# Performance work log

Measured on AMD Instinct MI355X. Metric: run time of the kernel, lower is better.

The kernel has to match this reference:

```python
import jax, jax.numpy as jnp
import numpy as np

B, T, F, H = 64, 512, 512, 1024


def setup_inputs() -> dict:
    key = jax.random.key(0)
    k1, k2, k3 = jax.random.split(key, 3)
    x = jax.random.normal(k1, (B, T, F), dtype=jnp.float32)
    c0 = jnp.zeros((B, H), dtype=jnp.float32)
    h0 = jnp.zeros((B, H), dtype=jnp.float32)
    # Flax LSTMCell: input projection (no bias) + hidden projection (with bias),
    # fused here into [4H]-wide kernels with gate order (i, f, g, o).
    Wi = jax.random.normal(k2, (F, 4 * H), dtype=jnp.float32) / np.sqrt(F)
    Wh = jax.random.normal(k3, (H, 4 * H), dtype=jnp.float32) / np.sqrt(H)
    bh = jnp.zeros((4 * H,), dtype=jnp.float32)
    return {"x": x, "c0": c0, "h0": h0, "Wi": Wi, "Wh": Wh, "bh": bh}


def reference(x, c0, h0, Wi, Wh, bh):
    # Precompute input projections for the whole sequence in one big GEMM.
    # zx: (T, B, 4H)
    zx = jnp.einsum('btf,fg->tbg', x, Wi)

    def step(carry, zx_t):
        c, h = carry
        z = zx_t + h @ Wh + bh  # (B, 4H)
        i, f, g, o = jnp.split(z, 4, axis=-1)
        i = jax.nn.sigmoid(i)
        f = jax.nn.sigmoid(f)
        g = jnp.tanh(g)
        o = jax.nn.sigmoid(o)
        c_new = f * c + i * g
        h_new = o * jnp.tanh(c_new)
        return (c_new, h_new), h_new

    (_, _), ys = jax.lax.scan(step, (c0, h0), zx)
    return jnp.swapaxes(ys, 0, 1)  # (B, T, H)
```

## Files before the change

kernel.cpp:

```cpp
#include <hip/hip_runtime.h>

#define Bdim 64
#define Tdim 512
#define Fdim 512
#define Hdim 1024
#define NKB  48
#define NXKB 16
#define NHKB 32
#define NWG  128
#define NTHR 256

typedef __attribute__((ext_vector_type(8))) _Float16     f16x8;
typedef __attribute__((ext_vector_type(4))) float        f32x4;
typedef __attribute__((ext_vector_type(4))) unsigned int u32x4;

#define MFMA(a, b, c) __builtin_amdgcn_mfma_f32_16x16x32_f16((a), (b), (c), 0, 0, 0)

#define WP_ELEMS    (256*48*64*8)
#define BIAS_OFF    ((size_t)WP_ELEMS * 2)
#define HBUF_OFF    (BIAS_OFF + 4096 * 4)
#define SLOT_BYTES  131072
#define NRING       513
#define FLAG_OFF    (HBUF_OFF + (size_t)NRING * SLOT_BYTES)
#define FLAG_STRIDE 32

__device__ __forceinline__ float sigmoidf_(float v) {
    return 1.0f / (1.0f + __expf(-v));
}
__device__ __forceinline__ float tanhf_(float v) {
    return 1.0f - 2.0f / (1.0f + __expf(2.0f * v));
}

__device__ __forceinline__ f16x8 uload16_l2(const void* p) {
    f16x8 r;
    asm volatile("global_load_dwordx4 %0, %1, off sc0"
                 : "=v"(r) : "v"(p) : "memory");
    return r;
}
__device__ __forceinline__ void ustore16(void* p, f32x4 v) {
    asm volatile("global_store_dwordx4 %0, %1, off sc0 sc1"
                 :: "v"(p), "v"(v) : "memory");
}

#define WAITV(N) do { asm volatile("s_waitcnt vmcnt(" #N ")" ::: "memory"); \
                      __builtin_amdgcn_sched_barrier(0); } while (0)

__global__ void pack_w_kernel(const float* __restrict__ Wi, const float* __restrict__ Wh,
                              _Float16* __restrict__ Wp)
{
    int d = blockIdx.x * blockDim.x + threadIdx.x;
    int tn   = d / 3072;
    int r    = d % 3072;
    int kb   = r / 64;
    int lane = r % 64;
    int kg = lane >> 4, lm = lane & 15;
    int Np = tn * 16 + lm;
    int g    = Np >> 5;
    int lc   = Np & 31;
    int gate = lc >> 3, c = lc & 7;
    int n  = gate * Hdim + g * 8 + c;
    int k0 = kb * 32 + kg * 8;
    f16x8 v;
#pragma unroll
    for (int j = 0; j < 8; ++j) {
        int k = k0 + j;
        float w = (k < Fdim) ? Wi[(long)k * 4096 + n] : Wh[(long)(k - Fdim) * 4096 + n];
        v[j] = (_Float16)w;
    }
    ((f16x8*)Wp)[d] = v;
}

__global__ void pack_misc_kernel(const float* __restrict__ bh, const float* __restrict__ h0,
                                 float* __restrict__ bias_p, _Float16* __restrict__ hbuf,
                                 unsigned int* __restrict__ flags)
{
    int t = blockIdx.x * blockDim.x + threadIdx.x;
    if (t < NWG) flags[t * FLAG_STRIDE] = 0u;
    if (t < 4096) {
        int g = t >> 5, lc = t & 31;
        int gate = lc >> 3, c = lc & 7;
        bias_p[t] = bh[gate * Hdim + g * 8 + c];
    }
    {
        int wgp = t >> 9;
        int b   = (t >> 3) & 63;
        int c   = t & 7;
        hbuf[t] = (_Float16)h0[b * Hdim + wgp * 8 + c];
    }
}

__global__ __launch_bounds__(NTHR, 1)
void lstm_kernel(const float* __restrict__ x, const float* __restrict__ c0,
                 const f16x8* __restrict__ Wp8, const float* __restrict__ bias_p,
                 _Float16* __restrict__ hbuf, unsigned int* __restrict__ flags,
                 float* __restrict__ out)
{
    __shared__ f16x8 wlds[2 * NKB * 64];
    __shared__ float zlds[Bdim][33];

    const int wg   = (blockIdx.x & 7) * 16 + (blockIdx.x >> 3);
    const int tid  = threadIdx.x;
    const int wave = tid >> 6;
    const int lane = tid & 63;
    const int kg = lane >> 4;
    const int lm = lane & 15;

    {
        const f16x8* src = Wp8 + (size_t)wg * 2 * NKB * 64;
        for (int e = tid; e < 2 * NKB * 64; e += NTHR) wlds[e] = src[e];
    }

    const float bias0 = bias_p[wg * 32 + lm];
    const float bias1 = bias_p[wg * 32 + 16 + lm];

    const int grow = wave * 16 + (lane >> 2);
    const int gjl  = (lane & 3) * 2;
    float cc0 = c0[grow * Hdim + wg * 8 + gjl];
    float cc1 = c0[grow * Hdim + wg * 8 + gjl + 1];

    const int arow = wave * 16 + lm;
    const float* __restrict__ xrow = x + (size_t)arow * Tdim * Fdim + kg * 8;

    char* __restrict__ hb  = (char*)hbuf;
    const char* __restrict__ hrd = hb + (size_t)kg * 1024 + (size_t)arow * 16;
    const size_t mypkt = (size_t)wg * 1024 + (size_t)grow * 16;

    __syncthreads();

    for (int t = 0; t < Tdim; ++t) {
        const unsigned int gen = (unsigned int)t;

        f32x4 acc0a = {bias0, bias0, bias0, bias0};
        f32x4 acc1a = {bias1, bias1, bias1, bias1};
        f32x4 acc0b = {0.f, 0.f, 0.f, 0.f};
        f32x4 acc1b = {0.f, 0.f, 0.f, 0.f};

        {
            const float* xt = xrow + (size_t)t * Fdim;
#pragma unroll 8
            for (int kb = 0; kb < NXKB; ++kb) {
                const f32x4* ap = (const f32x4*)(xt + kb * 32);
                f32x4 lo = ap[0];
                f32x4 hi = ap[1];
                f16x8 a;
#pragma unroll
                for (int j = 0; j < 4; ++j) { a[j] = (_Float16)lo[j]; a[4 + j] = (_Float16)hi[j]; }
                f16x8 bf0 = wlds[kb * 64 + lane];
                f16x8 bf1 = wlds[NKB * 64 + kb * 64 + lane];
                if (kb & 1) { acc0b = MFMA(a, bf0, acc0b); acc1b = MFMA(a, bf1, acc1b); }
                else        { acc0a = MFMA(a, bf0, acc0a); acc1a = MFMA(a, bf1, acc1a); }
            }
        }

        if (t && wave == 0) {
            const unsigned int target = 4u * gen;
            while (true) {
                unsigned int f0 = __hip_atomic_load(flags + (size_t)lane * FLAG_STRIDE,
                                                    __ATOMIC_RELAXED, __HIP_MEMORY_SCOPE_AGENT);
                unsigned int f1 = __hip_atomic_load(flags + (size_t)(64 + lane) * FLAG_STRIDE,
                                                    __ATOMIC_RELAXED, __HIP_MEMORY_SCOPE_AGENT);
                if (__all(f0 >= target && f1 >= target)) break;
                __builtin_amdgcn_s_sleep(1);
            }
        }
        __syncthreads();

        {
            const char* hq = hrd + (size_t)t * SLOT_BYTES;
            f16x8 hA[8], hB[8];

#define HLOAD(BASE, H)                                                  \
            _Pragma("unroll")                                           \
            for (int k = 0; k < 8; ++k)                                 \
                H[k] = uload16_l2(hq + (size_t)((BASE) + k) * 4096);

#define HGROUP(BASE, H)                                                 \
            _Pragma("unroll")                                           \
            for (int k = 0; k < 8; ++k) {                               \
                int kb = (BASE) + k;                                    \
                f16x8 bf0 = wlds[(NXKB + kb) * 64 + lane];              \
                f16x8 bf1 = wlds[NKB * 64 + (NXKB + kb) * 64 + lane];   \
                if (kb & 1) { acc0b = MFMA(H[k], bf0, acc0b); acc1b = MFMA(H[k], bf1, acc1b); } \
                else        { acc0a = MFMA(H[k], bf0, acc0a); acc1a = MFMA(H[k], bf1, acc1a); } \
            }

            HLOAD(0,  hA);
            HLOAD(8,  hB);
            WAITV(8);
            HGROUP(0,  hA);
            HLOAD(16, hA);
            WAITV(8);
            HGROUP(8,  hB);
            HLOAD(24, hB);
            WAITV(8);
            HGROUP(16, hA);
            WAITV(0);
            HGROUP(24, hB);
#undef HLOAD
#undef HGROUP
        }
        f32x4 z0 = acc0a + acc0b;
        f32x4 z1 = acc1a + acc1b;

        {
            int rbase = wave * 16 + kg * 4;
#pragma unroll
            for (int r = 0; r < 4; ++r) {
                zlds[rbase + r][lm]      = z0[r];
                zlds[rbase + r][16 + lm] = z1[r];
            }
        }
        asm volatile("s_waitcnt lgkmcnt(0)" ::: "memory");
        __builtin_amdgcn_sched_barrier(0);

        float hv0, hv1;
        {
            float i0 = sigmoidf_(zlds[grow][gjl]);
            float f0 = sigmoidf_(zlds[grow][8 + gjl]);
            float g0 = tanhf_(zlds[grow][16 + gjl]);
            float o0 = sigmoidf_(zlds[grow][24 + gjl]);
            cc0 = f0 * cc0 + i0 * g0;
            hv0 = o0 * tanhf_(cc0);

            float i1 = sigmoidf_(zlds[grow][gjl + 1]);
            float f1 = sigmoidf_(zlds[grow][8 + gjl + 1]);
            float g1 = tanhf_(zlds[grow][16 + gjl + 1]);
            float o1 = sigmoidf_(zlds[grow][24 + gjl + 1]);
            cc1 = f1 * cc1 + i1 * g1;
            hv1 = o1 * tanhf_(cc1);
        }

        {
            union { _Float16 h[2]; unsigned int u; } pk;
            pk.h[0] = (_Float16)hv0; pk.h[1] = (_Float16)hv1;
            const int lb = lane & ~3;
            unsigned int q0 = __shfl(pk.u, lb);
            unsigned int q1 = __shfl(pk.u, lb + 1);
            unsigned int q2 = __shfl(pk.u, lb + 2);
            unsigned int q3 = __shfl(pk.u, lb + 3);
            if (!(lane & 3)) {
                u32x4 pkt = {q0, q1, q2, q3};
                ustore16(hb + (size_t)(t + 1) * SLOT_BYTES + mypkt,
                         __builtin_bit_cast(f32x4, pkt));
            }
        }
        asm volatile("s_waitcnt vmcnt(0)" ::: "memory");
        if (lane == 0)
            __hip_atomic_fetch_add(flags + (size_t)wg * FLAG_STRIDE, 1u,
                                   __ATOMIC_RELAXED, __HIP_MEMORY_SCOPE_AGENT);

        {
            float2 ov; ov.x = hv0; ov.y = hv1;
            *(float2*)(out + ((size_t)grow * Tdim + t) * Hdim + wg * 8 + gjl) = ov;
        }
    }
}

extern "C" void kernel_launch(void* const* d_in, const int* in_sizes, int n_in,
                              void* d_out, int out_size, void* d_ws, size_t ws_size,
                              hipStream_t stream)
{
    const float* x  = (const float*)d_in[0];
    const float* c0 = (const float*)d_in[1];
    const float* h0 = (const float*)d_in[2];
    const float* Wi = (const float*)d_in[3];
    const float* Wh = (const float*)d_in[4];
    const float* bh = (const float*)d_in[5];
    float* out = (float*)d_out;

    char* ws = (char*)d_ws;
    _Float16*     Wp     = (_Float16*)(ws);
    float*        bias_p = (float*)(ws + BIAS_OFF);
    _Float16*     hbuf   = (_Float16*)(ws + HBUF_OFF);
    unsigned int* flags  = (unsigned int*)(ws + FLAG_OFF);

    hipLaunchKernelGGL(pack_w_kernel,    dim3(3072), dim3(256), 0, stream, Wi, Wh, Wp);
    hipLaunchKernelGGL(pack_misc_kernel, dim3(256),  dim3(256), 0, stream, bh, h0, bias_p, hbuf, flags);
    hipLaunchKernelGGL(lstm_kernel, dim3(NWG), dim3(NTHR), 0, stream,
                       x, c0, (const f16x8*)Wp, bias_p, hbuf, flags, out);
}
```

Baseline: 3.380 ms.

## Split each workgroup's gate tiles across eight waves instead of four

Workgroup size goes from 256 to 512 threads. Each wave now computes one 16-column gate tile for a 16-row block, rather than both tiles, so the serial MFMA chain per wave each timestep is halved. The gate nonlinearities are remapped to one hidden unit per lane, and an added barrier covers the cross-wave exchange through shared memory. The completion-flag target becomes 8 per step to match the wave count. In exchange, the x and h fragments are now loaded by two waves each, and there is an extra workgroup barrier every timestep.

```diff
diff --git a/kernel.cpp b/kernel.cpp
--- a/kernel.cpp
+++ b/kernel.cpp
@@ -8,7 +8,7 @@
 #define NXKB 16
 #define NHKB 32
 #define NWG  128
-#define NTHR 256
+#define NTHR 512
 
 typedef __attribute__((ext_vector_type(8))) _Float16     f16x8;
 typedef __attribute__((ext_vector_type(4))) float        f32x4;
@@ -98,27 +98,28 @@
     __shared__ f16x8 wlds[2 * NKB * 64];
     __shared__ float zlds[Bdim][33];
 
-    const int wg   = (blockIdx.x & 7) * 16 + (blockIdx.x >> 3);
-    const int tid  = threadIdx.x;
-    const int wave = tid >> 6;
-    const int lane = tid & 63;
-    const int kg = lane >> 4;
-    const int lm = lane & 15;
+    const int wg    = (blockIdx.x & 7) * 16 + (blockIdx.x >> 3);
+    const int tid   = threadIdx.x;
+    const int wave  = tid >> 6;
+    const int lane  = tid & 63;
+    const int kg    = lane >> 4;
+    const int lm    = lane & 15;
+    const int rtile = wave >> 1;
+    const int ctile = wave & 1;
 
     {
         const f16x8* src = Wp8 + (size_t)wg * 2 * NKB * 64;
         for (int e = tid; e < 2 * NKB * 64; e += NTHR) wlds[e] = src[e];
     }
 
-    const float bias0 = bias_p[wg * 32 + lm];
-    const float bias1 = bias_p[wg * 32 + 16 + lm];
-
-    const int grow = wave * 16 + (lane >> 2);
-    const int gjl  = (lane & 3) * 2;
-    float cc0 = c0[grow * Hdim + wg * 8 + gjl];
-    float cc1 = c0[grow * Hdim + wg * 8 + gjl + 1];
-
-    const int arow = wave * 16 + lm;
+    const float bias = bias_p[wg * 32 + ctile * 16 + lm];
+    const int   woff = ctile * (NKB * 64);
+
+    const int grow = wave * 8 + (lane >> 3);
+    const int gcol = lane & 7;
+    float cc = c0[grow * Hdim + wg * 8 + gcol];
+
+    const int arow = rtile * 16 + lm;
     const float* __restrict__ xrow = x + (size_t)arow * Tdim * Fdim + kg * 8;
 
     char* __restrict__ hb  = (char*)hbuf;
@@ -130,10 +131,8 @@
     for (int t = 0; t < Tdim; ++t) {
         const unsigned int gen = (unsigned int)t;
 
-        f32x4 acc0a = {bias0, bias0, bias0, bias0};
-        f32x4 acc1a = {bias1, bias1, bias1, bias1};
-        f32x4 acc0b = {0.f, 0.f, 0.f, 0.f};
-        f32x4 acc1b = {0.f, 0.f, 0.f, 0.f};
+        f32x4 acca = {bias, bias, bias, bias};
+        f32x4 accb = {0.f, 0.f, 0.f, 0.f};
 
         {
             const float* xt = xrow + (size_t)t * Fdim;
@@ -145,15 +144,14 @@
                 f16x8 a;
 #pragma unroll
                 for (int j = 0; j < 4; ++j) { a[j] = (_Float16)lo[j]; a[4 + j] = (_Float16)hi[j]; }
-                f16x8 bf0 = wlds[kb * 64 + lane];
-                f16x8 bf1 = wlds[NKB * 64 + kb * 64 + lane];
-                if (kb & 1) { acc0b = MFMA(a, bf0, acc0b); acc1b = MFMA(a, bf1, acc1b); }
-                else        { acc0a = MFMA(a, bf0, acc0a); acc1a = MFMA(a, bf1, acc1a); }
+                f16x8 bf = wlds[woff + kb * 64 + lane];
+                if (kb & 1) accb = MFMA(a, bf, accb);
+                else        acca = MFMA(a, bf, acca);
             }
         }
 
         if (t && wave == 0) {
-            const unsigned int target = 4u * gen;
+            const unsigned int target = 8u * gen;
             while (true) {
                 unsigned int f0 = __hip_atomic_load(flags + (size_t)lane * FLAG_STRIDE,
                                                     __ATOMIC_RELAXED, __HIP_MEMORY_SCOPE_AGENT);
@@ -163,7 +161,7 @@
                 __builtin_amdgcn_s_sleep(1);
             }
         }
-        __syncthreads();
+        __builtin_amdgcn_s_barrier();
 
         {
             const char* hq = hrd + (size_t)t * SLOT_BYTES;
@@ -178,10 +176,9 @@
             _Pragma("unroll")                                           \
             for (int k = 0; k < 8; ++k) {                               \
                 int kb = (BASE) + k;                                    \
-                f16x8 bf0 = wlds[(NXKB + kb) * 64 + lane];              \
-                f16x8 bf1 = wlds[NKB * 64 + (NXKB + kb) * 64 + lane];   \
-                if (kb & 1) { acc0b = MFMA(H[k], bf0, acc0b); acc1b = MFMA(H[k], bf1, acc1b); } \
-                else        { acc0a = MFMA(H[k], bf0, acc0a); acc1a = MFMA(H[k], bf1, acc1a); } \
+                f16x8 bf = wlds[woff + (NXKB + kb) * 64 + lane];        \
+                if (kb & 1) accb = MFMA(H[k], bf, accb);                \
+                else        acca = MFMA(H[k], bf, acca);                \
             }
 
             HLOAD(0,  hA);
@@ -199,46 +196,37 @@
 #undef HLOAD
 #undef HGROUP
         }
-        f32x4 z0 = acc0a + acc0b;
-        f32x4 z1 = acc1a + acc1b;
-
-        {
-            int rbase = wave * 16 + kg * 4;
+        f32x4 z = acca + accb;
+
+        {
+            int rbase = rtile * 16 + kg * 4;
 #pragma unroll
-            for (int r = 0; r < 4; ++r) {
-                zlds[rbase + r][lm]      = z0[r];
-                zlds[rbase + r][16 + lm] = z1[r];
-            }
+            for (int r = 0; r < 4; ++r)
+                zlds[rbase + r][ctile * 16 + lm] = z[r];
         }
         asm volatile("s_waitcnt lgkmcnt(0)" ::: "memory");
-        __builtin_amdgcn_sched_barrier(0);
-
-        float hv0, hv1;
-        {
-            float i0 = sigmoidf_(zlds[grow][gjl]);
-            float f0 = sigmoidf_(zlds[grow][8 + gjl]);
-            float g0 = tanhf_(zlds[grow][16 + gjl]);
-            float o0 = sigmoidf_(zlds[grow][24 + gjl]);
-            cc0 = f0 * cc0 + i0 * g0;
-            hv0 = o0 * tanhf_(cc0);
-
-            float i1 = sigmoidf_(zlds[grow][gjl + 1]);
-            float f1 = sigmoidf_(zlds[grow][8 + gjl + 1]);
-            float g1 = tanhf_(zlds[grow][16 + gjl + 1]);
-            float o1 = sigmoidf_(zlds[grow][24 + gjl + 1]);
-            cc1 = f1 * cc1 + i1 * g1;
-            hv1 = o1 * tanhf_(cc1);
-        }
-
-        {
-            union { _Float16 h[2]; unsigned int u; } pk;
-            pk.h[0] = (_Float16)hv0; pk.h[1] = (_Float16)hv1;
-            const int lb = lane & ~3;
-            unsigned int q0 = __shfl(pk.u, lb);
-            unsigned int q1 = __shfl(pk.u, lb + 1);
-            unsigned int q2 = __shfl(pk.u, lb + 2);
-            unsigned int q3 = __shfl(pk.u, lb + 3);
-            if (!(lane & 3)) {
+        __builtin_amdgcn_s_barrier();
+
+        float hv;
+        {
+            float ig = sigmoidf_(zlds[grow][gcol]);
+            float fg = sigmoidf_(zlds[grow][8 + gcol]);
+            float gg = tanhf_(zlds[grow][16 + gcol]);
+            float og = sigmoidf_(zlds[grow][24 + gcol]);
+            cc = fg * cc + ig * gg;
+            hv = og * tanhf_(cc);
+        }
+
+        {
+            union { _Float16 h; unsigned short u; } cv;
+            cv.h = (_Float16)hv;
+            unsigned int pk = cv.u;
+            const int lb = lane & ~7;
+            unsigned int q0 = __shfl(pk, lb)     | (__shfl(pk, lb + 1) << 16);
+            unsigned int q1 = __shfl(pk, lb + 2) | (__shfl(pk, lb + 3) << 16);
+            unsigned int q2 = __shfl(pk, lb + 4) | (__shfl(pk, lb + 5) << 16);
+            unsigned int q3 = __shfl(pk, lb + 6) | (__shfl(pk, lb + 7) << 16);
+            if (!(lane & 7)) {
                 u32x4 pkt = {q0, q1, q2, q3};
                 ustore16(hb + (size_t)(t + 1) * SLOT_BYTES + mypkt,
                          __builtin_bit_cast(f32x4, pkt));
@@ -249,10 +237,7 @@
             __hip_atomic_fetch_add(flags + (size_t)wg * FLAG_STRIDE, 1u,
                                    __ATOMIC_RELAXED, __HIP_MEMORY_SCOPE_AGENT);
 
-        {
-            float2 ov; ov.x = hv0; ov.y = hv1;
-            *(float2*)(out + ((size_t)grow * Tdim + t) * Hdim + wg * 8 + gjl) = ov;
-        }
+        out[((size_t)grow * Tdim + t) * Hdim + wg * 8 + gcol] = hv;
     }
 }
 
```

Result: slower. 5.371 ms (+58.9%).

## Specialize waves: dedicated waves prefetch the next step's input projection and poll flags

Applied to the files above, without the earlier changes.

The block grows to 8 waves. Four waves do the recurrent h·Wh MFMAs, the gate math and the h publish. The other four compute the x·Wi projection for the next timestep into a double-buffered LDS tile and spin on the cross-workgroup flags. The H waves then add the precomputed projection from LDS instead of computing it inline. This moves the input GEMM off the per-step serial path, at the cost of more threads per block, extra LDS traffic and a handoff through a block barrier.

```diff
diff --git a/kernel.cpp b/kernel.cpp
--- a/kernel.cpp
+++ b/kernel.cpp
@@ -8,7 +8,7 @@
 #define NXKB 16
 #define NHKB 32
 #define NWG  128
-#define NTHR 256
+#define NTHR 512
 
 typedef __attribute__((ext_vector_type(8))) _Float16     f16x8;
 typedef __attribute__((ext_vector_type(4))) float        f32x4;
@@ -97,13 +97,16 @@
 {
     __shared__ f16x8 wlds[2 * NKB * 64];
     __shared__ float zlds[Bdim][33];
-
-    const int wg   = (blockIdx.x & 7) * 16 + (blockIdx.x >> 3);
-    const int tid  = threadIdx.x;
-    const int wave = tid >> 6;
-    const int lane = tid & 63;
-    const int kg = lane >> 4;
-    const int lm = lane & 15;
+    __shared__ float zxlds[2][Bdim][33];
+
+    const int wg    = (blockIdx.x & 7) * 16 + (blockIdx.x >> 3);
+    const int tid   = threadIdx.x;
+    const int wave  = tid >> 6;
+    const int lane  = tid & 63;
+    const int kg    = lane >> 4;
+    const int lm    = lane & 15;
+    const bool isH  = (wave < 4);
+    const int  rt   = isH ? wave : (wave - 4);
 
     {
         const f16x8* src = Wp8 + (size_t)wg * 2 * NKB * 64;
@@ -113,147 +116,165 @@
     const float bias0 = bias_p[wg * 32 + lm];
     const float bias1 = bias_p[wg * 32 + 16 + lm];
 
-    const int grow = wave * 16 + (lane >> 2);
+    const int grow = (wave & 3) * 16 + (lane >> 2);
     const int gjl  = (lane & 3) * 2;
-    float cc0 = c0[grow * Hdim + wg * 8 + gjl];
-    float cc1 = c0[grow * Hdim + wg * 8 + gjl + 1];
-
-    const int arow = wave * 16 + lm;
+    float cc0 = 0.f, cc1 = 0.f;
+    if (isH) {
+        cc0 = c0[grow * Hdim + wg * 8 + gjl];
+        cc1 = c0[grow * Hdim + wg * 8 + gjl + 1];
+    }
+
+    const int arow = rt * 16 + lm;
     const float* __restrict__ xrow = x + (size_t)arow * Tdim * Fdim + kg * 8;
 
     char* __restrict__ hb  = (char*)hbuf;
     const char* __restrict__ hrd = hb + (size_t)kg * 1024 + (size_t)arow * 16;
     const size_t mypkt = (size_t)wg * 1024 + (size_t)grow * 16;
 
+#define XPHASE(TT, BUF)                                                     \
+    {                                                                       \
+        const float* xt = xrow + (size_t)(TT) * Fdim;                       \
+        f32x4 xa0 = {0.f, 0.f, 0.f, 0.f};                                   \
+        f32x4 xa1 = {0.f, 0.f, 0.f, 0.f};                                   \
+        _Pragma("unroll 8")                                                 \
+        for (int kb = 0; kb < NXKB; ++kb) {                                 \
+            const f32x4* ap = (const f32x4*)(xt + kb * 32);                 \
+            f32x4 lo = ap[0];                                               \
+            f32x4 hi = ap[1];                                               \
+            f16x8 a;                                                        \
+            _Pragma("unroll")                                               \
+            for (int j = 0; j < 4; ++j) { a[j] = (_Float16)lo[j]; a[4+j] = (_Float16)hi[j]; } \
+            xa0 = MFMA(a, wlds[kb * 64 + lane], xa0);                       \
+            xa1 = MFMA(a, wlds[NKB * 64 + kb * 64 + lane], xa1);            \
+        }                                                                   \
+        int rbase = rt * 16 + kg * 4;                                       \
+        _Pragma("unroll")                                                   \
+        for (int r = 0; r < 4; ++r) {                                       \
+            zxlds[BUF][rbase + r][lm]      = xa0[r];                        \
+            zxlds[BUF][rbase + r][16 + lm] = xa1[r];                        \
+        }                                                                   \
+    }
+
+    if (!isH) XPHASE(0, 0);
     __syncthreads();
 
     for (int t = 0; t < Tdim; ++t) {
-        const unsigned int gen = (unsigned int)t;
-
-        f32x4 acc0a = {bias0, bias0, bias0, bias0};
-        f32x4 acc1a = {bias1, bias1, bias1, bias1};
-        f32x4 acc0b = {0.f, 0.f, 0.f, 0.f};
-        f32x4 acc1b = {0.f, 0.f, 0.f, 0.f};
-
-        {
-            const float* xt = xrow + (size_t)t * Fdim;
-#pragma unroll 8
-            for (int kb = 0; kb < NXKB; ++kb) {
-                const f32x4* ap = (const f32x4*)(xt + kb * 32);
-                f32x4 lo = ap[0];
-                f32x4 hi = ap[1];
-                f16x8 a;
-#pragma unroll
-                for (int j = 0; j < 4; ++j) { a[j] = (_Float16)lo[j]; a[4 + j] = (_Float16)hi[j]; }
-                f16x8 bf0 = wlds[kb * 64 + lane];
-                f16x8 bf1 = wlds[NKB * 64 + kb * 64 + lane];
-                if (kb & 1) { acc0b = MFMA(a, bf0, acc0b); acc1b = MFMA(a, bf1, acc1b); }
-                else        { acc0a = MFMA(a, bf0, acc0a); acc1a = MFMA(a, bf1, acc1a); }
-            }
-        }
-
-        if (t && wave == 0) {
-            const unsigned int target = 4u * gen;
-            while (true) {
-                unsigned int f0 = __hip_atomic_load(flags + (size_t)lane * FLAG_STRIDE,
-                                                    __ATOMIC_RELAXED, __HIP_MEMORY_SCOPE_AGENT);
-                unsigned int f1 = __hip_atomic_load(flags + (size_t)(64 + lane) * FLAG_STRIDE,
-                                                    __ATOMIC_RELAXED, __HIP_MEMORY_SCOPE_AGENT);
-                if (__all(f0 >= target && f1 >= target)) break;
-                __builtin_amdgcn_s_sleep(1);
-            }
-        }
-        __syncthreads();
-
-        {
-            const char* hq = hrd + (size_t)t * SLOT_BYTES;
-            f16x8 hA[8], hB[8];
+        if (isH) {
+            f32x4 acc0a = {bias0, bias0, bias0, bias0};
+            f32x4 acc1a = {bias1, bias1, bias1, bias1};
+            f32x4 acc0b = {0.f, 0.f, 0.f, 0.f};
+            f32x4 acc1b = {0.f, 0.f, 0.f, 0.f};
+            {
+                const char* hq = hrd + (size_t)t * SLOT_BYTES;
+                f16x8 hA[8], hB[8];
 
 #define HLOAD(BASE, H)                                                  \
-            _Pragma("unroll")                                           \
-            for (int k = 0; k < 8; ++k)                                 \
-                H[k] = uload16_l2(hq + (size_t)((BASE) + k) * 4096);
+                _Pragma("unroll")                                       \
+                for (int k = 0; k < 8; ++k)                             \
+                    H[k] = uload16_l2(hq + (size_t)((BASE) + k) * 4096);
 
 #define HGROUP(BASE, H)                                                 \
-            _Pragma("unroll")                                           \
-            for (int k = 0; k < 8; ++k) {                               \
-                int kb = (BASE) + k;                                    \
-                f16x8 bf0 = wlds[(NXKB + kb) * 64 + lane];              \
-                f16x8 bf1 = wlds[NKB * 64 + (NXKB + kb) * 64 + lane];   \
-                if (kb & 1) { acc0b = MFMA(H[k], bf0, acc0b); acc1b = MFMA(H[k], bf1, acc1b); } \
-                else        { acc0a = MFMA(H[k], bf0, acc0a); acc1a = MFMA(H[k], bf1, acc1a); } \
-            }
-
-            HLOAD(0,  hA);
-            HLOAD(8,  hB);
-            WAITV(8);
-            HGROUP(0,  hA);
-            HLOAD(16, hA);
-            WAITV(8);
-            HGROUP(8,  hB);
-            HLOAD(24, hB);
-            WAITV(8);
-            HGROUP(16, hA);
-            WAITV(0);
-            HGROUP(24, hB);
+                _Pragma("unroll")                                       \
+                for (int k = 0; k < 8; ++k) {                           \
+                    int kb = (BASE) + k;                                \
+                    f16x8 bf0 = wlds[(NXKB + kb) * 64 + lane];          \
+                    f16x8 bf1 = wlds[NKB * 64 + (NXKB + kb) * 64 + lane]; \
+                    if (kb & 1) { acc0b = MFMA(H[k], bf0, acc0b); acc1b = MFMA(H[k], bf1, acc1b); } \
+                    else        { acc0a = MFMA(H[k], bf0, acc0a); acc1a = MFMA(H[k], bf1, acc1a); } \
+                }
+
+                HLOAD(0,  hA);
+                HLOAD(8,  hB);
+                WAITV(8);
+                HGROUP(0,  hA);
+                HLOAD(16, hA);
+                WAITV(8);
+                HGROUP(8,  hB);
+                HLOAD(24, hB);
+                WAITV(8);
+                HGROUP(16, hA);
+                WAITV(0);
+                HGROUP(24, hB);
 #undef HLOAD
 #undef HGROUP
+            }
+            {
+                const int buf = t & 1;
+                int rbase = rt * 16 + kg * 4;
+#pragma unroll
+                for (int r = 0; r < 4; ++r) {
+                    float z0 = acc0a[r] + acc0b[r] + zxlds[buf][rbase + r][lm];
+                    float z1 = acc1a[r] + acc1b[r] + zxlds[buf][rbase + r][16 + lm];
+                    zlds[rbase + r][lm]      = z0;
+                    zlds[rbase + r][16 + lm] = z1;
+                }
+            }
+            asm volatile("s_waitcnt lgkmcnt(0)" ::: "memory");
+            __builtin_amdgcn_sched_barrier(0);
+
+            float hv0, hv1;
+            {
+                float i0 = sigmoidf_(zlds[grow][gjl]);
+                float f0 = sigmoidf_(zlds[grow][8 + gjl]);
+                float g0 = tanhf_(zlds[grow][16 + gjl]);
+                float o0 = sigmoidf_(zlds[grow][24 + gjl]);
+                cc0 = f0 * cc0 + i0 * g0;
+                hv0 = o0 * tanhf_(cc0);
+
+                float i1 = sigmoidf_(zlds[grow][gjl + 1]);
+                float f1 = sigmoidf_(zlds[grow][8 + gjl + 1]);
+                float g1 = tanhf_(zlds[grow][16 + gjl + 1]);
+                float o1 = sigmoidf_(zlds[grow][24 + gjl + 1]);
+                cc1 = f1 * cc1 + i1 * g1;
+                hv1 = o1 * tanhf_(cc1);
+            }
+
+            {
+                union { _Float16 h[2]; unsigned int u; } pk;
+                pk.h[0] = (_Float16)hv0; pk.h[1] = (_Float16)hv1;
+                const int lb = lane & ~3;
+                unsigned int q0 = __shfl(pk.u, lb);
+                unsigned int q1 = __shfl(pk.u, lb + 1);
+                unsigned int q2 = __shfl(pk.u, lb + 2);
+                unsigned int q3 = __shfl(pk.u, lb + 3);
+                if (!(lane & 3)) {
+                    u32x4 pkt = {q0, q1, q2, q3};
+                    ustore16(hb + (size_t)(t + 1) * SLOT_BYTES + mypkt,
+                             __builtin_bit_cast(f32x4, pkt));
+                }
+            }
+            asm volatile("s_waitcnt vmcnt(0)" ::: "memory");
+            if (lane == 0)
+                __hip_atomic_fetch_add(flags + (size_t)wg * FLAG_STRIDE, 1u,
+                                       __ATOMIC_RELAXED, __HIP_MEMORY_SCOPE_AGENT);
+
+            {
+                float2 ov; ov.x = hv0; ov.y = hv1;
+                *(float2*)(out + ((size_t)grow * Tdim + t) * Hdim + wg * 8 + gjl) = ov;
+            }
+        } else {
+            {
+                const int tn  = (t + 1 < Tdim) ? (t + 1) : t;
+                const int buf = (t + 1) & 1;
+                XPHASE(tn, buf);
+            }
+            asm volatile("s_waitcnt lgkmcnt(0)" ::: "memory");
+
+            if (wave == 4 && t + 1 < Tdim) {
+                const unsigned int target = 4u * (unsigned int)(t + 1);
+                while (true) {
+                    unsigned int f0 = __hip_atomic_load(flags + (size_t)lane * FLAG_STRIDE,
+                                                        __ATOMIC_RELAXED, __HIP_MEMORY_SCOPE_AGENT);
+                    unsigned int f1 = __hip_atomic_load(flags + (size_t)(64 + lane) * FLAG_STRIDE,
+                                                        __ATOMIC_RELAXED, __HIP_MEMORY_SCOPE_AGENT);
+                    if (__all(f0 >= target && f1 >= target)) break;
+                    __builtin_amdgcn_s_sleep(1);
+                }
+            }
         }
-        f32x4 z0 = acc0a + acc0b;
-        f32x4 z1 = acc1a + acc1b;
-
-        {
-            int rbase = wave * 16 + kg * 4;
-#pragma unroll
-            for (int r = 0; r < 4; ++r) {
-                zlds[rbase + r][lm]      = z0[r];
-                zlds[rbase + r][16 + lm] = z1[r];
-            }
-        }
-        asm volatile("s_waitcnt lgkmcnt(0)" ::: "memory");
-        __builtin_amdgcn_sched_barrier(0);
-
-        float hv0, hv1;
-        {
-            float i0 = sigmoidf_(zlds[grow][gjl]);
-            float f0 = sigmoidf_(zlds[grow][8 + gjl]);
-            float g0 = tanhf_(zlds[grow][16 + gjl]);
-            float o0 = sigmoidf_(zlds[grow][24 + gjl]);
-            cc0 = f0 * cc0 + i0 * g0;
-            hv0 = o0 * tanhf_(cc0);
-
-            float i1 = sigmoidf_(zlds[grow][gjl + 1]);
-            float f1 = sigmoidf_(zlds[grow][8 + gjl + 1]);
-            float g1 = tanhf_(zlds[grow][16 + gjl + 1]);
-            float o1 = sigmoidf_(zlds[grow][24 + gjl + 1]);
-            cc1 = f1 * cc1 + i1 * g1;
-            hv1 = o1 * tanhf_(cc1);
-        }
-
-        {
-            union { _Float16 h[2]; unsigned int u; } pk;
-            pk.h[0] = (_Float16)hv0; pk.h[1] = (_Float16)hv1;
-            const int lb = lane & ~3;
-            unsigned int q0 = __shfl(pk.u, lb);
-            unsigned int q1 = __shfl(pk.u, lb + 1);
-            unsigned int q2 = __shfl(pk.u, lb + 2);
-            unsigned int q3 = __shfl(pk.u, lb + 3);
-            if (!(lane & 3)) {
-                u32x4 pkt = {q0, q1, q2, q3};
-                ustore16(hb + (size_t)(t + 1) * SLOT_BYTES + mypkt,
-                         __builtin_bit_cast(f32x4, pkt));
-            }
-        }
-        asm volatile("s_waitcnt vmcnt(0)" ::: "memory");
-        if (lane == 0)
-            __hip_atomic_fetch_add(flags + (size_t)wg * FLAG_STRIDE, 1u,
-                                   __ATOMIC_RELAXED, __HIP_MEMORY_SCOPE_AGENT);
-
-        {
-            float2 ov; ov.x = hv0; ov.y = hv1;
-            *(float2*)(out + ((size_t)grow * Tdim + t) * Hdim + wg * 8 + gjl) = ov;
-        }
-    }
+        __builtin_amdgcn_s_barrier();
+    }
+#undef XPHASE
 }
 
 extern "C" void kernel_launch(void* const* d_in, const int* in_sizes, int n_in,
```

New measurement: 3.329 ms. No clear change (-1.5%).
